# Kernel optimization log

Measured on AMD Instinct MI355X. Metric: run time of the kernel, lower is better.

Reference implementation:

```python
import jax, jax.numpy as jnp
import numpy as np


def setup_inputs() -> dict:
    key = jax.random.key(0)
    ks = jax.random.split(key, 5)
    B, C, H, W = 8, 64, 64, 64
    Ci = 32  # inter_channels = in_channels // 2
    s = 1.0 / np.sqrt(C)
    return {
        "x": jax.random.normal(ks[0], (B, C, H, W), jnp.float32),
        "Wg": jax.random.normal(ks[1], (Ci, C), jnp.float32) * s,
        "bg": jnp.zeros((Ci,), jnp.float32),
        "Wt": jax.random.normal(ks[2], (Ci, C), jnp.float32) * s,
        "bt": jnp.zeros((Ci,), jnp.float32),
        "Wp": jax.random.normal(ks[3], (Ci, C), jnp.float32) * s,
        "bp": jnp.zeros((Ci,), jnp.float32),
        "Ww": jax.random.normal(ks[4], (C, Ci), jnp.float32) * (1.0 / np.sqrt(Ci)),
        "bw": jnp.zeros((C,), jnp.float32),
    }


def _proj(x, Wc, bc):
    # 1x1 conv: (B,C,H,W) -> (B,O,H,W), then flatten spatial -> (B,O,N)
    b, c, h, w = x.shape
    y = jnp.einsum("oc,bchw->bohw", Wc, x) + bc[None, :, None, None]
    return y.reshape(b, Wc.shape[0], h * w)


def reference(x, Wg, bg, Wt, bt, Wp, bp, Ww, bw):
    b, c, h, w = x.shape
    g_x = _proj(x, Wg, bg).transpose(0, 2, 1)      # (B, N, Ci)
    theta_x = _proj(x, Wt, bt).transpose(0, 2, 1)  # (B, N, Ci)
    phi_x = _proj(x, Wp, bp)                        # (B, Ci, N)
    f = jnp.einsum("bnd,bdm->bnm", theta_x, phi_x)  # (B, N, N)
    f_div_C = jax.nn.softmax(f, axis=-1)
    y = jnp.einsum("bnm,bmd->bnd", f_div_C, g_x)    # (B, N, Ci)
    y = y.transpose(0, 2, 1).reshape(b, Wg.shape[0], h, w)
    W_y = jnp.einsum("od,bdhw->bohw", Ww, y) + bw[None, :, None, None]
    return W_y + x
```

## Files before the change

### kernel.cpp

```cpp
#include <hip/hip_runtime.h>
#include <hip/hip_bf16.h>
#include <cstdint>
#include <cstddef>

#define B_ 8
#define C_ 64
#define CI 32
#define N_ 4096
#define LOG2E 1.44269504088896340736f

typedef __attribute__((ext_vector_type(8))) short bf16x8;
typedef __attribute__((ext_vector_type(4))) float f32x4;

static __device__ __forceinline__ ushort f2bf(float x) {
  union { float f; uint32_t u; } v; v.f = x;
  uint32_t r = v.u + 0x7FFFu + ((v.u >> 16) & 1u);
  return (ushort)(r >> 16);
}

static __device__ __forceinline__ uint32_t cvt_pk_bf16(float lo, float hi) {
  uint32_t r;
  asm("v_cvt_pk_bf16_f32 %0, %1, %2" : "=v"(r) : "v"(lo), "v"(hi));
  return r;
}

__global__ __launch_bounds__(256) void proj_kernel(
    const float* __restrict__ x,
    const float* __restrict__ Wg, const float* __restrict__ bg,
    const float* __restrict__ Wt, const float* __restrict__ bt,
    const float* __restrict__ Wp, const float* __restrict__ bp,
    ushort* __restrict__ theta_t, ushort* __restrict__ phi_t,
    ushort* __restrict__ gmat)
{
  __shared__ float WLt[C_ * CI];
  __shared__ float bL[CI];

  const int z = blockIdx.z;
  const float* W; const float* bias;
  if (z == 0)      { W = Wt; bias = bt; }
  else if (z == 1) { W = Wp; bias = bp; }
  else             { W = Wg; bias = bg; }

  const int t = threadIdx.x;
  #pragma unroll
  for (int k = 0; k < 8; ++k) {
    const int i = t + k * 256;
    WLt[(i % C_) * CI + (i / C_)] = W[i];
  }
  if (t < CI) bL[t] = bias[t];
  __syncthreads();

  const int b = blockIdx.y;
  const int n = blockIdx.x * 64 + (t & 63);
  const int dq = t >> 6;
  const float* xb = x + ((size_t)b * C_) * N_ + n;

  float acc[8];
  #pragma unroll
  for (int i = 0; i < 8; ++i) acc[i] = bL[dq * 8 + i];

  #pragma unroll 8
  for (int c = 0; c < C_; ++c) {
    const float xv = xb[(size_t)c * N_];
    const float4 w0 = *(const float4*)&WLt[c * CI + dq * 8];
    const float4 w1 = *(const float4*)&WLt[c * CI + dq * 8 + 4];
    acc[0] = fmaf(w0.x, xv, acc[0]);
    acc[1] = fmaf(w0.y, xv, acc[1]);
    acc[2] = fmaf(w0.z, xv, acc[2]);
    acc[3] = fmaf(w0.w, xv, acc[3]);
    acc[4] = fmaf(w1.x, xv, acc[4]);
    acc[5] = fmaf(w1.y, xv, acc[5]);
    acc[6] = fmaf(w1.z, xv, acc[6]);
    acc[7] = fmaf(w1.w, xv, acc[7]);
  }

  if (z == 2) {
    #pragma unroll
    for (int i = 0; i < 8; ++i)
      gmat[((size_t)(b * CI) + dq * 8 + i) * N_ + n] = f2bf(acc[i]);
  } else {
    const float scale = (z == 0) ? LOG2E : 1.0f;
    uint32_t w[4];
    #pragma unroll
    for (int k = 0; k < 4; ++k)
      w[k] = (uint32_t)f2bf(acc[2 * k] * scale) |
             ((uint32_t)f2bf(acc[2 * k + 1] * scale) << 16);
    ushort* base = (z == 0) ? theta_t : phi_t;
    *(uint4*)(base + ((size_t)(b * N_) + n) * CI + dq * 8) =
        make_uint4(w[0], w[1], w[2], w[3]);
  }
}

__global__ __launch_bounds__(512, 2) void attn_kernel(
    const ushort* __restrict__ theta_t,
    const ushort* __restrict__ phi_t,
    const ushort* __restrict__ gmat,
    const float* __restrict__ Ww, const float* __restrict__ bw,
    const float* __restrict__ x, float* __restrict__ out)
{
  __shared__ union {
    ushort pt[8][2][16 * 64];
    float  accS[4][32][64];
  } Sh;
  __shared__ float mlS[4][8][64];
  __shared__ float WwL[C_ * CI];
  __shared__ float Yl[32 * 66];

  const int tid = threadIdx.x;
  const int lane = tid & 63;
  const int mh = tid >> 6;
  const int bid = blockIdx.x;
  const int b = bid & 7;
  const int n0 = (bid >> 3) * 64;
  const int g4 = lane >> 4;
  const int c16 = lane & 15;
  const int sw = (c16 & 7) << 4;

  #pragma unroll
  for (int i = 0; i < 4; ++i) WwL[tid + i * 512] = Ww[tid + i * 512];

  bf16x8 qfrag[4];
  #pragma unroll
  for (int s = 0; s < 4; ++s)
    qfrag[s] = *(const bf16x8*)(theta_t +
        ((size_t)(b * N_ + n0 + s * 16 + c16)) * CI + g4 * 8);

  f32x4 acc[4][2];
  f32x4 cinit[4];
  #pragma unroll
  for (int s = 0; s < 4; ++s) {
    acc[s][0] = (f32x4){0.f, 0.f, 0.f, 0.f};
    acc[s][1] = (f32x4){0.f, 0.f, 0.f, 0.f};
    cinit[s]  = (f32x4){0.f, 0.f, 0.f, 0.f};
  }
  float l_lane[4] = {0.f, 0.f, 0.f, 0.f};

  const int mq0 = mh * 512;
  const ushort* kbase = phi_t + ((size_t)(b * N_ + mq0 + c16)) * CI + g4 * 8;
  const ushort* vb0 = gmat + ((size_t)(b * CI + c16)) * N_ + mq0 + g4 * 8;
  const ushort* vb1 = vb0 + (size_t)16 * N_;

  char* pw[2][4]; const char* prd[2][2];
  #pragma unroll
  for (int pb = 0; pb < 2; ++pb) {
    #pragma unroll
    for (int mt = 0; mt < 4; ++mt)
      pw[pb][mt] = (char*)Sh.pt[mh][pb] + ((c16 * 128 + mt * 32 + g4 * 8) ^ sw);
    #pragma unroll
    for (int ks = 0; ks < 2; ++ks)
      prd[pb][ks] = (const char*)Sh.pt[mh][pb] +
                    ((c16 * 128 + ks * 64 + g4 * 16) ^ sw);
  }

  bf16x8 kf[4], kfn[4], vf0[2], vf1[2];
  #pragma unroll
  for (int mt = 0; mt < 4; ++mt)
    kfn[mt] = *(const bf16x8*)(kbase + (size_t)(mt * 16) * CI);

  const int NT = 8;
  for (int t = 0; t < NT; ++t) {
    #pragma unroll
    for (int mt = 0; mt < 4; ++mt) kf[mt] = kfn[mt];
    const int tn = (t + 1 < NT) ? t + 1 : t;
    #pragma unroll
    for (int mt = 0; mt < 4; ++mt)
      kfn[mt] = *(const bf16x8*)(kbase + (size_t)(tn * 64 + mt * 16) * CI);
    #pragma unroll
    for (int ks = 0; ks < 2; ++ks) {
      vf0[ks] = *(const bf16x8*)(vb0 + t * 64 + ks * 32);
      vf1[ks] = *(const bf16x8*)(vb1 + t * 64 + ks * 32);
    }

    #pragma unroll
    for (int s = 0; s < 4; ++s) {
      const int pb = s & 1;
      f32x4 f[4];
      __builtin_amdgcn_s_setprio(1);
      #pragma unroll
      for (int mt = 0; mt < 4; ++mt)
        f[mt] = __builtin_amdgcn_mfma_f32_16x16x32_bf16(
            kf[mt], qfrag[s], cinit[s], 0, 0, 0);
      __builtin_amdgcn_s_setprio(0);

      float pv[4][4];
      #pragma unroll
      for (int mt = 0; mt < 4; ++mt) {
        #pragma unroll
        for (int rr = 0; rr < 4; ++rr)
          pv[mt][rr] = __builtin_amdgcn_exp2f(f[mt][rr]);
        l_lane[s] += (pv[mt][0] + pv[mt][1]) + (pv[mt][2] + pv[mt][3]);
      }
      #pragma unroll
      for (int mt = 0; mt < 4; ++mt) {
        uint2 wv;
        wv.x = cvt_pk_bf16(pv[mt][0], pv[mt][1]);
        wv.y = cvt_pk_bf16(pv[mt][2], pv[mt][3]);
        *(uint2*)pw[pb][mt] = wv;
      }
      asm volatile("s_waitcnt lgkmcnt(0)" ::: "memory");
      __builtin_amdgcn_sched_barrier(0);

      __builtin_amdgcn_s_setprio(1);
      #pragma unroll
      for (int ks = 0; ks < 2; ++ks) {
        const bf16x8 pfrag = *(const bf16x8*)prd[pb][ks];
        acc[s][0] = __builtin_amdgcn_mfma_f32_16x16x32_bf16(
            vf0[ks], pfrag, acc[s][0], 0, 0, 0);
        acc[s][1] = __builtin_amdgcn_mfma_f32_16x16x32_bf16(
            vf1[ks], pfrag, acc[s][1], 0, 0, 0);
      }
      __builtin_amdgcn_s_setprio(0);

      if (__any(l_lane[s] > 0x1p40f)) {
        const float sc = 0x1p-64f;
        acc[s][0] *= sc; acc[s][1] *= sc; l_lane[s] *= sc;
        #pragma unroll
        for (int rr = 0; rr < 4; ++rr) cinit[s][rr] -= 64.f;
      }
    }
  }

  float m_run[4];
  #pragma unroll
  for (int s = 0; s < 4; ++s) {
    l_lane[s] += __shfl_xor(l_lane[s], 16);
    l_lane[s] += __shfl_xor(l_lane[s], 32);
    m_run[s] = -cinit[s][0];
  }

  #pragma unroll
  for (int r = 4; r >= 1; r >>= 1) {
    __syncthreads();
    if (mh >= r && mh < 2 * r) {
      float* ad = &Sh.accS[mh - r][0][0] + lane;
      float* md = &mlS[mh - r][0][0] + lane;
      #pragma unroll
      for (int s = 0; s < 4; ++s) {
        #pragma unroll
        for (int rr = 0; rr < 4; ++rr) {
          ad[(s * 8 + rr) * 64]     = acc[s][0][rr];
          ad[(s * 8 + 4 + rr) * 64] = acc[s][1][rr];
        }
        md[s * 64]       = m_run[s];
        md[(4 + s) * 64] = l_lane[s];
      }
    }
    __syncthreads();
    if (mh < r) {
      const float* as_ = &Sh.accS[mh][0][0] + lane;
      const float* ms_ = &mlS[mh][0][0] + lane;
      #pragma unroll
      for (int s = 0; s < 4; ++s) {
        const float mb = ms_[s * 64];
        const float lb = ms_[(4 + s) * 64];
        const float mM = fmaxf(m_run[s], mb);
        const float ea = __builtin_amdgcn_exp2f(m_run[s] - mM);
        const float eb = __builtin_amdgcn_exp2f(mb - mM);
        #pragma unroll
        for (int rr = 0; rr < 4; ++rr) {
          acc[s][0][rr] = acc[s][0][rr] * ea + as_[(s * 8 + rr) * 64] * eb;
          acc[s][1][rr] = acc[s][1][rr] * ea + as_[(s * 8 + 4 + rr) * 64] * eb;
        }
        l_lane[s] = l_lane[s] * ea + lb * eb;
        m_run[s] = mM;
      }
    }
  }
  __syncthreads();

  if (mh == 0) {
    #pragma unroll
    for (int s = 0; s < 4; ++s) {
      const float inv = 1.0f / l_lane[s];
      const int q = s * 16 + c16;
      #pragma unroll
      for (int rr = 0; rr < 4; ++rr) {
        Yl[(g4 * 4 + rr) * 66 + q]      = acc[s][0][rr] * inv;
        Yl[(16 + g4 * 4 + rr) * 66 + q] = acc[s][1][rr] * inv;
      }
    }
  }
  __syncthreads();

  const int nl = tid & 63;
  const int cg = tid >> 6;
  float oacc[8];
  #pragma unroll
  for (int i = 0; i < 8; ++i) oacc[i] = bw[cg * 8 + i];
  #pragma unroll
  for (int d = 0; d < CI; ++d) {
    const float yv = Yl[d * 66 + nl];
    #pragma unroll
    for (int i = 0; i < 8; ++i)
      oacc[i] = fmaf(WwL[(cg * 8 + i) * CI + d], yv, oacc[i]);
  }
  #pragma unroll
  for (int i = 0; i < 8; ++i) {
    const size_t idx = ((size_t)(b * C_ + cg * 8 + i)) * N_ + n0 + nl;
    out[idx] = oacc[i] + x[idx];
  }
}

extern "C" void kernel_launch(void* const* d_in, const int* in_sizes, int n_in,
                              void* d_out, int out_size, void* d_ws, size_t ws_size,
                              hipStream_t stream) {
  const float* x  = (const float*)d_in[0];
  const float* Wg = (const float*)d_in[1];
  const float* bg = (const float*)d_in[2];
  const float* Wt = (const float*)d_in[3];
  const float* bt = (const float*)d_in[4];
  const float* Wp = (const float*)d_in[5];
  const float* bp = (const float*)d_in[6];
  const float* Ww = (const float*)d_in[7];
  const float* bw = (const float*)d_in[8];
  float* out = (float*)d_out;

  char* ws = (char*)d_ws;
  ushort* theta_t = (ushort*)(ws);
  ushort* phi_t   = (ushort*)(ws + (size_t)2 * 1024 * 1024);
  ushort* gmat    = (ushort*)(ws + (size_t)4 * 1024 * 1024);

  proj_kernel<<<dim3(N_ / 64, B_, 3), 256, 0, stream>>>(
      x, Wg, bg, Wt, bt, Wp, bp, theta_t, phi_t, gmat);
  attn_kernel<<<dim3((N_ / 64) * B_), 512, 0, stream>>>(
      theta_t, phi_t, gmat, Ww, bw, x, out);
}
```

Baseline: 60.36 us.

## Switch attention to 32x32x16 MFMA and pass P through lane shuffles instead of LDS

Rewrites the attention inner loop to use 32x32x16 bf16 MFMA tiles (two query tiles of 32) instead of 16x16x32 tiles. The softmax probabilities are now re-laid out into the B-operand format with cross-half-wave shuffles rather than a round trip through shared memory with waitcnt barriers. This is meant to remove the LDS write/read latency and its synchronisation between the two GEMMs. The trade-offs are that K-fragment prefetching is dropped and the running-max subtraction is now an explicit branch. Register pressure also changes with the 16-wide accumulators.

```diff
diff --git a/kernel.cpp b/kernel.cpp
--- a/kernel.cpp
+++ b/kernel.cpp
@@ -11,6 +11,7 @@
 
 typedef __attribute__((ext_vector_type(8))) short bf16x8;
 typedef __attribute__((ext_vector_type(4))) float f32x4;
+typedef __attribute__((ext_vector_type(16))) float f32x16;
 
 static __device__ __forceinline__ ushort f2bf(float x) {
   union { float f; uint32_t u; } v; v.f = x;
@@ -98,11 +99,8 @@
     const float* __restrict__ Ww, const float* __restrict__ bw,
     const float* __restrict__ x, float* __restrict__ out)
 {
-  __shared__ union {
-    ushort pt[8][2][16 * 64];
-    float  accS[4][32][64];
-  } Sh;
-  __shared__ float mlS[4][8][64];
+  __shared__ float accS[4][32][64];
+  __shared__ float mlS[4][4][64];
   __shared__ float WwL[C_ * CI];
   __shared__ float Yl[32 * 66];
 
@@ -112,157 +110,150 @@
   const int bid = blockIdx.x;
   const int b = bid & 7;
   const int n0 = (bid >> 3) * 64;
-  const int g4 = lane >> 4;
-  const int c16 = lane & 15;
-  const int sw = (c16 & 7) << 4;
+  const int q32 = lane & 31;
+  const int h = lane >> 5;
 
   #pragma unroll
   for (int i = 0; i < 4; ++i) WwL[tid + i * 512] = Ww[tid + i * 512];
 
-  bf16x8 qfrag[4];
-  #pragma unroll
-  for (int s = 0; s < 4; ++s)
-    qfrag[s] = *(const bf16x8*)(theta_t +
-        ((size_t)(b * N_ + n0 + s * 16 + c16)) * CI + g4 * 8);
-
-  f32x4 acc[4][2];
-  f32x4 cinit[4];
-  #pragma unroll
-  for (int s = 0; s < 4; ++s) {
-    acc[s][0] = (f32x4){0.f, 0.f, 0.f, 0.f};
-    acc[s][1] = (f32x4){0.f, 0.f, 0.f, 0.f};
-    cinit[s]  = (f32x4){0.f, 0.f, 0.f, 0.f};
-  }
-  float l_lane[4] = {0.f, 0.f, 0.f, 0.f};
-
-  const int mq0 = mh * 512;
-  const ushort* kbase = phi_t + ((size_t)(b * N_ + mq0 + c16)) * CI + g4 * 8;
-  const ushort* vb0 = gmat + ((size_t)(b * CI + c16)) * N_ + mq0 + g4 * 8;
-  const ushort* vb1 = vb0 + (size_t)16 * N_;
-
-  char* pw[2][4]; const char* prd[2][2];
-  #pragma unroll
-  for (int pb = 0; pb < 2; ++pb) {
-    #pragma unroll
-    for (int mt = 0; mt < 4; ++mt)
-      pw[pb][mt] = (char*)Sh.pt[mh][pb] + ((c16 * 128 + mt * 32 + g4 * 8) ^ sw);
-    #pragma unroll
-    for (int ks = 0; ks < 2; ++ks)
-      prd[pb][ks] = (const char*)Sh.pt[mh][pb] +
-                    ((c16 * 128 + ks * 64 + g4 * 16) ^ sw);
-  }
-
-  bf16x8 kf[4], kfn[4], vf0[2], vf1[2];
-  #pragma unroll
-  for (int mt = 0; mt < 4; ++mt)
-    kfn[mt] = *(const bf16x8*)(kbase + (size_t)(mt * 16) * CI);
+  bf16x8 qf[2][2];
+  #pragma unroll
+  for (int qt = 0; qt < 2; ++qt)
+    #pragma unroll
+    for (int dh = 0; dh < 2; ++dh)
+      qf[qt][dh] = *(const bf16x8*)(theta_t +
+          ((size_t)(b * N_ + n0 + qt * 32 + q32)) * CI + dh * 16 + h * 8);
+
+  f32x16 acc[2];
+  #pragma unroll
+  for (int qt = 0; qt < 2; ++qt)
+    #pragma unroll
+    for (int r = 0; r < 16; ++r) acc[qt][r] = 0.f;
+  float m_run[2] = {0.f, 0.f};
+  float l_lane[2] = {0.f, 0.f};
+
+  const ushort* kf_base = phi_t + ((size_t)(b * N_ + mh * 512 + q32)) * CI + h * 8;
+  const ushort* vf_base = gmat + ((size_t)(b * CI + q32)) * N_ + mh * 512 + h * 8;
 
   const int NT = 8;
   for (int t = 0; t < NT; ++t) {
-    #pragma unroll
-    for (int mt = 0; mt < 4; ++mt) kf[mt] = kfn[mt];
-    const int tn = (t + 1 < NT) ? t + 1 : t;
-    #pragma unroll
-    for (int mt = 0; mt < 4; ++mt)
-      kfn[mt] = *(const bf16x8*)(kbase + (size_t)(tn * 64 + mt * 16) * CI);
-    #pragma unroll
-    for (int ks = 0; ks < 2; ++ks) {
-      vf0[ks] = *(const bf16x8*)(vb0 + t * 64 + ks * 32);
-      vf1[ks] = *(const bf16x8*)(vb1 + t * 64 + ks * 32);
-    }
-
-    #pragma unroll
-    for (int s = 0; s < 4; ++s) {
-      const int pb = s & 1;
-      f32x4 f[4];
-      __builtin_amdgcn_s_setprio(1);
+    bf16x8 vf[4];
+    #pragma unroll
+    for (int ks = 0; ks < 4; ++ks)
+      vf[ks] = *(const bf16x8*)(vf_base + t * 64 + ks * 16);
+
+    #pragma unroll
+    for (int msub = 0; msub < 2; ++msub) {
+      const bf16x8 kfA = *(const bf16x8*)(kf_base +
+          (size_t)(t * 64 + msub * 32) * CI);
+      const bf16x8 kfB = *(const bf16x8*)(kf_base +
+          (size_t)(t * 64 + msub * 32) * CI + 16);
+
       #pragma unroll
-      for (int mt = 0; mt < 4; ++mt)
-        f[mt] = __builtin_amdgcn_mfma_f32_16x16x32_bf16(
-            kf[mt], qfrag[s], cinit[s], 0, 0, 0);
-      __builtin_amdgcn_s_setprio(0);
-
-      float pv[4][4];
-      #pragma unroll
-      for (int mt = 0; mt < 4; ++mt) {
-        #pragma unroll
-        for (int rr = 0; rr < 4; ++rr)
-          pv[mt][rr] = __builtin_amdgcn_exp2f(f[mt][rr]);
-        l_lane[s] += (pv[mt][0] + pv[mt][1]) + (pv[mt][2] + pv[mt][3]);
+      for (int qt = 0; qt < 2; ++qt) {
+        f32x16 z;
+        #pragma unroll
+        for (int r = 0; r < 16; ++r) z[r] = 0.f;
+        __builtin_amdgcn_s_setprio(1);
+        f32x16 f = __builtin_amdgcn_mfma_f32_32x32x16_bf16(
+            kfA, qf[qt][0], z, 0, 0, 0);
+        f = __builtin_amdgcn_mfma_f32_32x32x16_bf16(
+            kfB, qf[qt][1], f, 0, 0, 0);
+        __builtin_amdgcn_s_setprio(0);
+
+        float p[16];
+        if (m_run[qt] == 0.f) {
+          #pragma unroll
+          for (int r = 0; r < 16; ++r)
+            p[r] = __builtin_amdgcn_exp2f(f[r]);
+        } else {
+          #pragma unroll
+          for (int r = 0; r < 16; ++r)
+            p[r] = __builtin_amdgcn_exp2f(f[r] - m_run[qt]);
+        }
+        float ls = 0.f;
+        #pragma unroll
+        for (int r = 0; r < 16; r += 4)
+          ls += (p[r] + p[r + 1]) + (p[r + 2] + p[r + 3]);
+        l_lane[qt] += ls;
+
+        uint32_t w[8];
+        #pragma unroll
+        for (int j = 0; j < 8; ++j)
+          w[j] = cvt_pk_bf16(p[2 * j], p[2 * j + 1]);
+
+        const uint32_t s0 = h ? w[0] : w[2];
+        const uint32_t s1 = h ? w[1] : w[3];
+        const uint32_t s2 = h ? w[4] : w[6];
+        const uint32_t s3 = h ? w[5] : w[7];
+        const uint32_t r0 = (uint32_t)__shfl_xor((int)s0, 32, 64);
+        const uint32_t r1 = (uint32_t)__shfl_xor((int)s1, 32, 64);
+        const uint32_t r2 = (uint32_t)__shfl_xor((int)s2, 32, 64);
+        const uint32_t r3 = (uint32_t)__shfl_xor((int)s3, 32, 64);
+
+        union { uint32_t u[4]; bf16x8 v; } B0, B1;
+        B0.u[0] = h ? r0 : w[0];
+        B0.u[1] = h ? r1 : w[1];
+        B0.u[2] = h ? w[2] : r0;
+        B0.u[3] = h ? w[3] : r1;
+        B1.u[0] = h ? r2 : w[4];
+        B1.u[1] = h ? r3 : w[5];
+        B1.u[2] = h ? w[6] : r2;
+        B1.u[3] = h ? w[7] : r3;
+
+        __builtin_amdgcn_s_setprio(1);
+        acc[qt] = __builtin_amdgcn_mfma_f32_32x32x16_bf16(
+            vf[msub * 2], B0.v, acc[qt], 0, 0, 0);
+        acc[qt] = __builtin_amdgcn_mfma_f32_32x32x16_bf16(
+            vf[msub * 2 + 1], B1.v, acc[qt], 0, 0, 0);
+        __builtin_amdgcn_s_setprio(0);
       }
-      #pragma unroll
-      for (int mt = 0; mt < 4; ++mt) {
-        uint2 wv;
-        wv.x = cvt_pk_bf16(pv[mt][0], pv[mt][1]);
-        wv.y = cvt_pk_bf16(pv[mt][2], pv[mt][3]);
-        *(uint2*)pw[pb][mt] = wv;
+    }
+
+    #pragma unroll
+    for (int qt = 0; qt < 2; ++qt) {
+      if (__any(l_lane[qt] > 0x1p40f)) {
+        #pragma unroll
+        for (int r = 0; r < 16; ++r) acc[qt][r] *= 0x1p-64f;
+        l_lane[qt] *= 0x1p-64f;
+        m_run[qt] += 64.f;
       }
-      asm volatile("s_waitcnt lgkmcnt(0)" ::: "memory");
-      __builtin_amdgcn_sched_barrier(0);
-
-      __builtin_amdgcn_s_setprio(1);
-      #pragma unroll
-      for (int ks = 0; ks < 2; ++ks) {
-        const bf16x8 pfrag = *(const bf16x8*)prd[pb][ks];
-        acc[s][0] = __builtin_amdgcn_mfma_f32_16x16x32_bf16(
-            vf0[ks], pfrag, acc[s][0], 0, 0, 0);
-        acc[s][1] = __builtin_amdgcn_mfma_f32_16x16x32_bf16(
-            vf1[ks], pfrag, acc[s][1], 0, 0, 0);
-      }
-      __builtin_amdgcn_s_setprio(0);
-
-      if (__any(l_lane[s] > 0x1p40f)) {
-        const float sc = 0x1p-64f;
-        acc[s][0] *= sc; acc[s][1] *= sc; l_lane[s] *= sc;
-        #pragma unroll
-        for (int rr = 0; rr < 4; ++rr) cinit[s][rr] -= 64.f;
-      }
-    }
-  }
-
-  float m_run[4];
-  #pragma unroll
-  for (int s = 0; s < 4; ++s) {
-    l_lane[s] += __shfl_xor(l_lane[s], 16);
-    l_lane[s] += __shfl_xor(l_lane[s], 32);
-    m_run[s] = -cinit[s][0];
-  }
+    }
+  }
+
+  #pragma unroll
+  for (int qt = 0; qt < 2; ++qt)
+    l_lane[qt] += __shfl_xor(l_lane[qt], 32, 64);
 
   #pragma unroll
   for (int r = 4; r >= 1; r >>= 1) {
     __syncthreads();
     if (mh >= r && mh < 2 * r) {
-      float* ad = &Sh.accS[mh - r][0][0] + lane;
-      float* md = &mlS[mh - r][0][0] + lane;
+      const int slot = mh - r;
       #pragma unroll
-      for (int s = 0; s < 4; ++s) {
-        #pragma unroll
-        for (int rr = 0; rr < 4; ++rr) {
-          ad[(s * 8 + rr) * 64]     = acc[s][0][rr];
-          ad[(s * 8 + 4 + rr) * 64] = acc[s][1][rr];
-        }
-        md[s * 64]       = m_run[s];
-        md[(4 + s) * 64] = l_lane[s];
-      }
+      for (int qt = 0; qt < 2; ++qt)
+        #pragma unroll
+        for (int rr = 0; rr < 16; ++rr)
+          accS[slot][qt * 16 + rr][lane] = acc[qt][rr];
+      mlS[slot][0][lane] = m_run[0];
+      mlS[slot][1][lane] = m_run[1];
+      mlS[slot][2][lane] = l_lane[0];
+      mlS[slot][3][lane] = l_lane[1];
     }
     __syncthreads();
     if (mh < r) {
-      const float* as_ = &Sh.accS[mh][0][0] + lane;
-      const float* ms_ = &mlS[mh][0][0] + lane;
       #pragma unroll
-      for (int s = 0; s < 4; ++s) {
-        const float mb = ms_[s * 64];
-        const float lb = ms_[(4 + s) * 64];
-        const float mM = fmaxf(m_run[s], mb);
-        const float ea = __builtin_amdgcn_exp2f(m_run[s] - mM);
+      for (int qt = 0; qt < 2; ++qt) {
+        const float mb = mlS[mh][qt][lane];
+        const float lb = mlS[mh][2 + qt][lane];
+        const float mM = fmaxf(m_run[qt], mb);
+        const float ea = __builtin_amdgcn_exp2f(m_run[qt] - mM);
         const float eb = __builtin_amdgcn_exp2f(mb - mM);
         #pragma unroll
-        for (int rr = 0; rr < 4; ++rr) {
-          acc[s][0][rr] = acc[s][0][rr] * ea + as_[(s * 8 + rr) * 64] * eb;
-          acc[s][1][rr] = acc[s][1][rr] * ea + as_[(s * 8 + 4 + rr) * 64] * eb;
-        }
-        l_lane[s] = l_lane[s] * ea + lb * eb;
-        m_run[s] = mM;
+        for (int rr = 0; rr < 16; ++rr)
+          acc[qt][rr] = acc[qt][rr] * ea + accS[mh][qt * 16 + rr][lane] * eb;
+        l_lane[qt] = l_lane[qt] * ea + lb * eb;
+        m_run[qt] = mM;
       }
     }
   }
@@ -270,13 +261,13 @@
 
   if (mh == 0) {
     #pragma unroll
-    for (int s = 0; s < 4; ++s) {
-      const float inv = 1.0f / l_lane[s];
-      const int q = s * 16 + c16;
+    for (int qt = 0; qt < 2; ++qt) {
+      const float inv = 1.0f / l_lane[qt];
+      const int q = qt * 32 + q32;
       #pragma unroll
-      for (int rr = 0; rr < 4; ++rr) {
-        Yl[(g4 * 4 + rr) * 66 + q]      = acc[s][0][rr] * inv;
-        Yl[(16 + g4 * 4 + rr) * 66 + q] = acc[s][1][rr] * inv;
+      for (int rr = 0; rr < 16; ++rr) {
+        const int d = (rr & 3) + 8 * (rr >> 2) + 4 * h;
+        Yl[d * 66 + q] = acc[qt][rr] * inv;
       }
     }
   }
```

After: 65.73 us. 1.09x slower.
